# Optimization experiments

Measured on AMD Instinct MI355X. Metric: run time of the kernel, lower is better.

The kernel has to match this reference:

```python
import jax, jax.numpy as jnp
import numpy as np

HID = 2048
NH = 16
HD = HID // NH  # 128
THETA = 10000.0


def _rope_cos_sin(position_ids):
    # inv_freq: [HD/2]
    inv_freq = 1.0 / (THETA ** (jnp.arange(0, HD, 2, dtype=jnp.float32) / HD))
    freqs = position_ids.astype(jnp.float32)[:, :, None] * inv_freq[None, None, :]  # [b,s,hd/2]
    emb = jnp.concatenate([freqs, freqs], axis=-1)  # [b,s,hd]
    return jnp.cos(emb), jnp.sin(emb)


def _rotate_half(x):
    x1, x2 = x[..., : HD // 2], x[..., HD // 2:]
    return jnp.concatenate([-x2, x1], axis=-1)


def setup_inputs() -> dict:
    key = jax.random.key(0)
    ks = jax.random.split(key, 10)
    b, s = 2, 2048
    scale = 1.0 / np.sqrt(HID)
    hidden_states = jax.random.normal(ks[0], (b, s, HID), dtype=jnp.float32)
    wq = jax.random.normal(ks[1], (HID, HID), dtype=jnp.float32) * scale
    wk = jax.random.normal(ks[2], (HID, HID), dtype=jnp.float32) * scale
    wv = jax.random.normal(ks[3], (HID, HID), dtype=jnp.float32) * scale
    wo = jax.random.normal(ks[4], (HID, HID), dtype=jnp.float32) * scale
    bq = jnp.zeros((HID,), jnp.float32)
    bk = jnp.zeros((HID,), jnp.float32)
    bv = jnp.zeros((HID,), jnp.float32)
    bo = jnp.zeros((HID,), jnp.float32)
    # HF-style additive causal mask [b,1,q,kv]: 0 on/below diag, large negative above
    neg = jnp.finfo(jnp.float32).min
    causal = jnp.where(jnp.tril(jnp.ones((s, s), dtype=bool)), 0.0, neg)
    attention_mask = jnp.broadcast_to(causal[None, None], (b, 1, s, s)).astype(jnp.float32)
    position_ids = jnp.broadcast_to(jnp.arange(s, dtype=jnp.int32)[None], (b, s))
    return {
        "hidden_states": hidden_states,
        "wq": wq, "bq": bq, "wk": wk, "bk": bk,
        "wv": wv, "bv": bv, "wo": wo, "bo": bo,
        "attention_mask": attention_mask, "position_ids": position_ids,
    }


def reference(hidden_states, wq, bq, wk, bk, wv, bv, wo, bo, attention_mask, position_ids):
    b, s, _ = hidden_states.shape
    q = hidden_states @ wq.T + bq  # [b,s,hid]
    k = hidden_states @ wk.T + bk
    v = hidden_states @ wv.T + bv
    # [b, nh, s, hd]
    q = q.reshape(b, s, NH, HD).transpose(0, 2, 1, 3)
    k = k.reshape(b, s, NH, HD).transpose(0, 2, 1, 3)
    v = v.reshape(b, s, NH, HD).transpose(0, 2, 1, 3)
    cos, sin = _rope_cos_sin(position_ids)  # [b,s,hd]
    cos, sin = cos[:, None], sin[:, None]  # unsqueeze_dim=1 -> [b,1,s,hd]
    q = q * cos + _rotate_half(q) * sin
    k = k * cos + _rotate_half(k) * sin
    scores = jnp.einsum("bhqd,bhkd->bhqk", q, k) / np.sqrt(HD)
    scores = scores + attention_mask
    attn = jax.nn.softmax(scores.astype(jnp.float32), axis=-1).astype(q.dtype)
    out = jnp.einsum("bhqk,bhkd->bhqd", attn, v)  # [b,nh,s,hd]
    out = out.transpose(0, 2, 1, 3).reshape(b, s, HID)
    return out @ wo.T + bo
```

## Files before the change

### kernel.cpp

```cpp
#include <hip/hip_runtime.h>

#define S_LEN 2048
#define HID   2048
#define NHEAD 16
#define HDIM  128
#define BATCH 2
#define KDIM  2048

using bf16x8  = __attribute__((ext_vector_type(8))) short;
using f32x4   = __attribute__((ext_vector_type(4))) float;
using short4v = __attribute__((ext_vector_type(4))) short;

__device__ __forceinline__ short f2bf(float f) {
  union { float f; unsigned u; } v; v.f = f;
  unsigned r = v.u + 0x7fffu + ((v.u >> 16) & 1u);
  return (short)(r >> 16);
}
__device__ __forceinline__ float bf2f(short s) {
  union { unsigned u; float f; } v;
  v.u = ((unsigned)(unsigned short)s) << 16;
  return v.f;
}

__device__ __forceinline__ void gl_lds16(const void* g, void* l) {
  __builtin_amdgcn_global_load_lds(
      (const __attribute__((address_space(1))) void*)g,
      (__attribute__((address_space(3))) void*)l, 16, 0, 0);
}

__global__ __launch_bounds__(256)
void convert_all(const float* __restrict__ hs, const float* __restrict__ wq,
                 const float* __restrict__ wk, const float* __restrict__ wv,
                 const float* __restrict__ wo,
                 short* __restrict__ hsb, short* __restrict__ wqkv,
                 short* __restrict__ wob)
{
  int i = blockIdx.x * 256 + threadIdx.x;
  const float* src; short* dst; int j = i;
  if (j < 1048576)      { src = hs; dst = hsb; }
  else if (j < 1572864) { j -= 1048576; src = wq; dst = wqkv; }
  else if (j < 2097152) { j -= 1572864; src = wk; dst = wqkv + 4194304; }
  else if (j < 2621440) { j -= 2097152; src = wv; dst = wqkv + 8388608; }
  else                  { j -= 2621440; src = wo; dst = wob; }
  f32x4 a = ((const f32x4*)src)[2 * j];
  f32x4 b = ((const f32x4*)src)[2 * j + 1];
  bf16x8 o;
  o[0]=f2bf(a[0]); o[1]=f2bf(a[1]); o[2]=f2bf(a[2]); o[3]=f2bf(a[3]);
  o[4]=f2bf(b[0]); o[5]=f2bf(b[1]); o[6]=f2bf(b[2]); o[7]=f2bf(b[3]);
  ((bf16x8*)dst)[j] = o;
}

template<int KIND>
__global__ __launch_bounds__(256)
void gemm128(const short* __restrict__ A, const short* __restrict__ B,
             const float* __restrict__ bias0, const float* __restrict__ bias1,
             const float* __restrict__ bias2,
             void* __restrict__ O0, void* __restrict__ O1, void* __restrict__ O2)
{
  __shared__ __align__(16) short As[128 * 64];
  __shared__ __align__(16) short Bs[128 * 64];
  const int tid  = threadIdx.x;
  const int lane = tid & 63, wave = tid >> 6;
  const int ln = lane & 15, g = lane >> 4;
  const int wr = wave >> 1, wc = wave & 1;
  const int m0 = blockIdx.x * 128, n0 = blockIdx.y * 128;

  const int srow   = tid >> 3;
  const int schunk = (tid & 7) ^ (srow & 7);
  const short* aS = A + (size_t)(m0 + srow) * KDIM + schunk * 8;
  const short* bS = B + (size_t)(n0 + srow) * KDIM + schunk * 8;

  f32x4 acc[4][4] = {};

  for (int k0 = 0; k0 < KDIM; k0 += 64) {
    __syncthreads();
#pragma unroll
    for (int j = 0; j < 4; ++j) {
      gl_lds16(aS + k0 + j * (32 * KDIM), &As[j * 2048 + tid * 8]);
      gl_lds16(bS + k0 + j * (32 * KDIM), &Bs[j * 2048 + tid * 8]);
    }
    __syncthreads();

#pragma unroll
    for (int ks = 0; ks < 2; ++ks) {
      bf16x8 af[4], bfm[4];
#pragma unroll
      for (int i = 0; i < 4; ++i) {
        const int r = wr * 64 + i * 16 + ln;
        af[i] = *(const bf16x8*)&As[r * 64 + (((ks * 4 + g) ^ (r & 7)) << 3)];
      }
#pragma unroll
      for (int j2 = 0; j2 < 4; ++j2) {
        const int r = wc * 64 + j2 * 16 + ln;
        bfm[j2] = *(const bf16x8*)&Bs[r * 64 + (((ks * 4 + g) ^ (r & 7)) << 3)];
      }
#pragma unroll
      for (int i = 0; i < 4; ++i)
#pragma unroll
        for (int j2 = 0; j2 < 4; ++j2)
          acc[i][j2] = __builtin_amdgcn_mfma_f32_16x16x32_bf16(af[i], bfm[j2], acc[i][j2], 0, 0, 0);
    }
  }

  if constexpr (KIND == 0) {
    const int seg   = n0 >> 11;
    const int nbase = (n0 & 2047) + wc * 64;
    const float* bias = (seg == 0) ? bias0 : (seg == 1) ? bias1 : bias2;
    float bvv[4];
#pragma unroll
    for (int j = 0; j < 4; ++j) bvv[j] = bias[nbase + j * 16 + ln];
    if (seg < 2) {
      short* C = (short*)(seg ? O1 : O0);
#pragma unroll
      for (int i = 0; i < 4; ++i) {
        const int mb = m0 + wr * 64 + i * 16 + 4 * g;
#pragma unroll
        for (int j = 0; j < 4; ++j) {
          const int nl = nbase + j * 16 + ln;
          const int h = nl >> 7, d = nl & 127;
#pragma unroll
          for (int e = 0; e < 4; ++e) {
            const int m = mb + e, bb = m >> 11, t = m & (S_LEN - 1);
            C[((size_t)((bb * NHEAD + h) * S_LEN + t) << 7) + d] = f2bf(acc[i][j][e] + bvv[j]);
          }
        }
      }
    } else {
      short* C = (short*)O2;
#pragma unroll
      for (int i = 0; i < 4; ++i) {
        const int mb = m0 + wr * 64 + i * 16 + 4 * g;
        const int bb = mb >> 11, t0 = mb & (S_LEN - 1);
#pragma unroll
        for (int j = 0; j < 4; ++j) {
          const int nl = nbase + j * 16 + ln;
          const int h = nl >> 7, d = nl & 127;
          short4v v;
#pragma unroll
          for (int e = 0; e < 4; ++e) v[e] = f2bf(acc[i][j][e] + bvv[j]);
          *(short4v*)&C[((size_t)((bb * NHEAD + h) * HDIM + d)) * S_LEN + t0] = v;
        }
      }
    }
  } else {
    float* C = (float*)O0;
    float bvv[4];
#pragma unroll
    for (int j = 0; j < 4; ++j) bvv[j] = bias0[n0 + wc * 64 + j * 16 + ln];
#pragma unroll
    for (int i = 0; i < 4; ++i) {
      const int mb = m0 + wr * 64 + i * 16 + 4 * g;
#pragma unroll
      for (int j = 0; j < 4; ++j) {
        const int n = n0 + wc * 64 + j * 16 + ln;
#pragma unroll
        for (int e = 0; e < 4; ++e)
          C[(size_t)(mb + e) * HID + n] = acc[i][j][e] + bvv[j];
      }
    }
  }
}

#define QSCALE 0.12752767502f
__global__ __launch_bounds__(256)
void rope_kernel(short* __restrict__ Qb, short* __restrict__ Kb,
                 const int* __restrict__ pos_ids)
{
  const int row = blockIdx.x * 4 + (threadIdx.x >> 6);
  const int d   = threadIdx.x & 63;
  const int bh  = row >> 11, t = row & (S_LEN - 1);
  const int b   = bh >> 4;
  const float pos = (float)pos_ids[b * S_LEN + t];
  const float inv = powf(10000.0f, -(float)d * (1.0f / 64.0f));
  float s, c;
  sincosf(pos * inv, &s, &c);
  const size_t base = (size_t)row * HDIM;
  {
    float x1 = bf2f(Qb[base + d]), x2 = bf2f(Qb[base + d + 64]);
    Qb[base + d]      = f2bf((x1 * c - x2 * s) * QSCALE);
    Qb[base + d + 64] = f2bf((x2 * c + x1 * s) * QSCALE);
  }
  {
    float x1 = bf2f(Kb[base + d]), x2 = bf2f(Kb[base + d + 64]);
    Kb[base + d]      = f2bf(x1 * c - x2 * s);
    Kb[base + d + 64] = f2bf(x2 * c + x1 * s);
  }
}

__global__ __launch_bounds__(512)
void attn_kernel(const short* __restrict__ Qb, const short* __restrict__ Kb,
                 const short* __restrict__ Vt, short* __restrict__ AO)
{
  __shared__ __align__(16) short Ks[64 * 128];
  __shared__ __align__(16) short Vs[128 * 64];
  __shared__ __align__(16) short Ps[8][16 * 64];
  const int tid  = threadIdx.x;
  const int wave = tid >> 6, lane = tid & 63;
  const int ln = lane & 15, g = lane >> 4;
  const int bid = blockIdx.x;
  const int bh  = bid & 31;
  const int grp = bid >> 5;
  const int yt  = (grp & 7) ^ ((grp & 8) ? 15 : 0);
  const int qw  = yt * 128 + wave * 16;

  bf16x8 qf[4];
#pragma unroll
  for (int ks = 0; ks < 4; ++ks)
    qf[ks] = *(const bf16x8*)&Qb[((size_t)bh * S_LEN + qw + ln) * HDIM + ks * 32 + g * 8];

  f32x4 o[8] = {};
  float m_e[4], l_e[4];
#pragma unroll
  for (int e = 0; e < 4; ++e) { m_e[e] = -3.0e38f; l_e[e] = 0.f; }

  const int kvt_max = 2 * yt + 1;
  for (int kvt = 0; kvt <= kvt_max; ++kvt) {
    const int kv0 = kvt * 64;
    __syncthreads();
#pragma unroll
    for (int p = 0; p < 2; ++p) {
      const int gi = tid + p * 512;
      {
        const int row = gi >> 4, c8 = gi & 15;
        bf16x8 v = *(const bf16x8*)&Kb[((size_t)bh * S_LEN + kv0 + row) * HDIM + c8 * 8];
        *(bf16x8*)&Ks[(row * 128 + c8 * 8) ^ ((row & 7) << 3)] = v;
      }
      {
        const int dr = gi >> 3, cg = gi & 7;
        bf16x8 v = *(const bf16x8*)&Vt[((size_t)bh * HDIM + dr) * S_LEN + kv0 + cg * 8];
        *(bf16x8*)&Vs[(dr * 64 + cg * 8) ^ ((dr & 7) << 3)] = v;
      }
    }
    __syncthreads();

    f32x4 sfr[4] = {};
    __builtin_amdgcn_s_setprio(1);
#pragma unroll
    for (int ks = 0; ks < 4; ++ks) {
#pragma unroll
      for (int nt = 0; nt < 4; ++nt) {
        const int row = nt * 16 + ln;
        bf16x8 kf = *(const bf16x8*)&Ks[(row * 128 + ks * 32 + g * 8) ^ ((ln & 7) << 3)];
        sfr[nt] = __builtin_amdgcn_mfma_f32_16x16x32_bf16(qf[ks], kf, sfr[nt], 0, 0, 0);
      }
    }
    __builtin_amdgcn_s_setprio(0);

    float rmax_e[4];
#pragma unroll
    for (int e = 0; e < 4; ++e) {
      const int q = qw + 4 * g + e;
      float rmax = -3.0e38f;
#pragma unroll
      for (int nt = 0; nt < 4; ++nt) {
        float v = sfr[nt][e];
        if (kv0 + nt * 16 + ln > q) v = -3.0e38f;
        sfr[nt][e] = v;
        rmax = fmaxf(rmax, v);
      }
#pragma unroll
      for (int msk = 1; msk < 16; msk <<= 1)
        rmax = fmaxf(rmax, __shfl_xor(rmax, msk));
      rmax_e[e] = rmax;
    }

    bool grow = false;
#pragma unroll
    for (int e = 0; e < 4; ++e) grow |= (rmax_e[e] > m_e[e] + 8.0f);
    if (__any(grow)) {
#pragma unroll
      for (int e = 0; e < 4; ++e) {
        const float nm = fmaxf(m_e[e], rmax_e[e]);
        const float corr = exp2f(m_e[e] - nm);
        m_e[e] = nm;
        l_e[e] *= corr;
#pragma unroll
        for (int nt2 = 0; nt2 < 8; ++nt2) o[nt2][e] *= corr;
      }
    }

#pragma unroll
    for (int e = 0; e < 4; ++e) {
      float psum = 0.f;
#pragma unroll
      for (int nt = 0; nt < 4; ++nt) {
        const float pv = exp2f(sfr[nt][e] - m_e[e]);
        sfr[nt][e] = pv;
        psum += pv;
      }
      l_e[e] += psum;
    }

    short* pw = &Ps[wave][0];
#pragma unroll
    for (int e = 0; e < 4; ++e) {
      const int r = 4 * g + e;
#pragma unroll
      for (int nt = 0; nt < 4; ++nt) {
        const int cc = nt * 16 + ln;
        pw[(r * 64 + cc) ^ ((r & 7) << 3)] = f2bf(sfr[nt][e]);
      }
    }
    asm volatile("s_waitcnt lgkmcnt(0)" ::: "memory");
    __builtin_amdgcn_sched_barrier(0);

    __builtin_amdgcn_s_setprio(1);
#pragma unroll
    for (int ks2 = 0; ks2 < 2; ++ks2) {
      bf16x8 pa = *(const bf16x8*)&pw[(ln * 64 + ks2 * 32 + g * 8) ^ ((ln & 7) << 3)];
#pragma unroll
      for (int nt2 = 0; nt2 < 8; ++nt2) {
        const int row = nt2 * 16 + ln;
        bf16x8 vb = *(const bf16x8*)&Vs[(row * 64 + ks2 * 32 + g * 8) ^ ((ln & 7) << 3)];
        o[nt2] = __builtin_amdgcn_mfma_f32_16x16x32_bf16(pa, vb, o[nt2], 0, 0, 0);
      }
    }
    __builtin_amdgcn_s_setprio(0);
  }

  const int b = bh >> 4, h = bh & 15;
#pragma unroll
  for (int e = 0; e < 4; ++e) {
    float l = l_e[e];
#pragma unroll
    for (int msk = 1; msk < 16; msk <<= 1)
      l += __shfl_xor(l, msk);
    const float inv = 1.0f / l;
    const int q = qw + 4 * g + e;
    short* dst = &AO[((size_t)b * S_LEN + q) * HID + h * HDIM];
#pragma unroll
    for (int nt2 = 0; nt2 < 8; ++nt2)
      dst[nt2 * 16 + ln] = f2bf(o[nt2][e] * inv);
  }
}

extern "C" void kernel_launch(void* const* d_in, const int* in_sizes, int n_in,
                              void* d_out, int out_size, void* d_ws, size_t ws_size,
                              hipStream_t stream)
{
  const float* hs = (const float*)d_in[0];
  const float* wq = (const float*)d_in[1];
  const float* bq = (const float*)d_in[2];
  const float* wk = (const float*)d_in[3];
  const float* bk = (const float*)d_in[4];
  const float* wv = (const float*)d_in[5];
  const float* bv = (const float*)d_in[6];
  const float* wo = (const float*)d_in[7];
  const float* bo = (const float*)d_in[8];
  const int*  pos = (const int*)d_in[10];
  float* out = (float*)d_out;

  const size_t TSZ = (size_t)BATCH * NHEAD * S_LEN * HDIM;
  short* Qb   = (short*)d_ws;
  short* Kb   = Qb + TSZ;
  short* Vt   = Kb + TSZ;
  short* hsb  = Vt + TSZ;
  short* AO   = hsb;
  short* Wqkv = hsb + TSZ;
  short* wob  = Wqkv + 12582912;

  convert_all<<<12288, 256, 0, stream>>>(hs, wq, wk, wv, wo, hsb, Wqkv, wob);
  gemm128<0><<<dim3(32, 48), 256, 0, stream>>>(hsb, Wqkv, bq, bk, bv, Qb, Kb, Vt);
  rope_kernel<<<(BATCH * NHEAD * S_LEN) / 4, 256, 0, stream>>>(Qb, Kb, pos);
  attn_kernel<<<512, 512, 0, stream>>>(Qb, Kb, Vt, AO);
  gemm128<1><<<dim3(32, 16), 256, 0, stream>>>(AO, wob, bo, nullptr, nullptr, out, nullptr, nullptr);
}
```

Baseline: 276.6 us.

## Double-buffer K/V tiles in attention with async global-to-LDS loads

The attention kernel now keeps two LDS buffers for K and V. It prefetches the next KV tile with direct global-to-LDS loads while the current tile is being computed, and uses vmcnt waits plus barriers in place of the synchronous load-then-sync pattern. The XOR swizzle is moved from the LDS destination into the global source address, which leaves the LDS layout unchanged. The aim is to hide global memory latency behind the MFMA work. The cost is double the K/V LDS footprint, which may reduce occupancy.

```diff
diff --git a/kernel.cpp b/kernel.cpp
--- a/kernel.cpp
+++ b/kernel.cpp
@@ -191,8 +191,8 @@
 void attn_kernel(const short* __restrict__ Qb, const short* __restrict__ Kb,
                  const short* __restrict__ Vt, short* __restrict__ AO)
 {
-  __shared__ __align__(16) short Ks[64 * 128];
-  __shared__ __align__(16) short Vs[128 * 64];
+  __shared__ __align__(16) short Ks[2][64 * 128];
+  __shared__ __align__(16) short Vs[2][128 * 64];
   __shared__ __align__(16) short Ps[8][16 * 64];
   const int tid  = threadIdx.x;
   const int wave = tid >> 6, lane = tid & 63;
@@ -203,6 +203,11 @@
   const int yt  = (grp & 7) ^ ((grp & 8) ? 15 : 0);
   const int qw  = yt * 128 + wave * 16;
 
+  const short* Kbh = Kb + (size_t)bh * (S_LEN * HDIM);
+  const short* Vbh = Vt + (size_t)bh * (S_LEN * HDIM);
+  const int kOff = (tid >> 4) * HDIM + (((tid & 15) ^ ((tid >> 4) & 7)) << 3);
+  const int vOff = (tid >> 3) * S_LEN + (((tid & 7) ^ ((tid >> 3) & 7)) << 3);
+
   bf16x8 qf[4];
 #pragma unroll
   for (int ks = 0; ks < 4; ++ks)
@@ -213,25 +218,30 @@
 #pragma unroll
   for (int e = 0; e < 4; ++e) { m_e[e] = -3.0e38f; l_e[e] = 0.f; }
 
+  auto stage = [&](int kvt, int b) {
+    const int kv0 = kvt * 64;
+    const short* ksrc = Kbh + (size_t)kv0 * HDIM + kOff;
+    const short* vsrc = Vbh + kv0 + vOff;
+    gl_lds16(ksrc,                 &Ks[b][tid * 8]);
+    gl_lds16(ksrc + 32 * HDIM,     &Ks[b][4096 + tid * 8]);
+    gl_lds16(vsrc,                 &Vs[b][tid * 8]);
+    gl_lds16(vsrc + 64 * S_LEN,    &Vs[b][4096 + tid * 8]);
+  };
+
+  stage(0, 0);
   const int kvt_max = 2 * yt + 1;
   for (int kvt = 0; kvt <= kvt_max; ++kvt) {
-    const int kv0 = kvt * 64;
-    __syncthreads();
-#pragma unroll
-    for (int p = 0; p < 2; ++p) {
-      const int gi = tid + p * 512;
-      {
-        const int row = gi >> 4, c8 = gi & 15;
-        bf16x8 v = *(const bf16x8*)&Kb[((size_t)bh * S_LEN + kv0 + row) * HDIM + c8 * 8];
-        *(bf16x8*)&Ks[(row * 128 + c8 * 8) ^ ((row & 7) << 3)] = v;
-      }
-      {
-        const int dr = gi >> 3, cg = gi & 7;
-        bf16x8 v = *(const bf16x8*)&Vt[((size_t)bh * HDIM + dr) * S_LEN + kv0 + cg * 8];
-        *(bf16x8*)&Vs[(dr * 64 + cg * 8) ^ ((dr & 7) << 3)] = v;
-      }
-    }
-    __syncthreads();
+    const int cur = kvt & 1;
+    if (kvt < kvt_max) {
+      stage(kvt + 1, cur ^ 1);
+      asm volatile("s_waitcnt vmcnt(4)" ::: "memory");
+    } else {
+      asm volatile("s_waitcnt vmcnt(0)" ::: "memory");
+    }
+    __builtin_amdgcn_s_barrier();
+    __builtin_amdgcn_sched_barrier(0);
+    const short* kb = &Ks[cur][0];
+    const short* vbuf = &Vs[cur][0];
 
     f32x4 sfr[4] = {};
     __builtin_amdgcn_s_setprio(1);
@@ -240,12 +250,13 @@
 #pragma unroll
       for (int nt = 0; nt < 4; ++nt) {
         const int row = nt * 16 + ln;
-        bf16x8 kf = *(const bf16x8*)&Ks[(row * 128 + ks * 32 + g * 8) ^ ((ln & 7) << 3)];
+        bf16x8 kf = *(const bf16x8*)&kb[(row * 128 + ks * 32 + g * 8) ^ ((ln & 7) << 3)];
         sfr[nt] = __builtin_amdgcn_mfma_f32_16x16x32_bf16(qf[ks], kf, sfr[nt], 0, 0, 0);
       }
     }
     __builtin_amdgcn_s_setprio(0);
 
+    const int kv0 = kvt * 64;
     float rmax_e[4];
 #pragma unroll
     for (int e = 0; e < 4; ++e) {
@@ -311,11 +322,14 @@
 #pragma unroll
       for (int nt2 = 0; nt2 < 8; ++nt2) {
         const int row = nt2 * 16 + ln;
-        bf16x8 vb = *(const bf16x8*)&Vs[(row * 64 + ks2 * 32 + g * 8) ^ ((ln & 7) << 3)];
+        bf16x8 vb = *(const bf16x8*)&vbuf[(row * 64 + ks2 * 32 + g * 8) ^ ((row & 7) << 3)];
         o[nt2] = __builtin_amdgcn_mfma_f32_16x16x32_bf16(pa, vb, o[nt2], 0, 0, 0);
       }
     }
     __builtin_amdgcn_s_setprio(0);
+
+    __builtin_amdgcn_sched_barrier(0);
+    __builtin_amdgcn_s_barrier();
   }
 
   const int b = bh >> 4, h = bh & 15;
```

New measurement: 275.4 us. About the same (-0.4%).

## Load 128-row KV tiles via direct global-to-LDS loads; loop convert kernel

Applied to the files above, without the earlier changes.

The attention kernel now stages 128-row K and V tiles per barrier pair using global_load_lds direct copies, with the XOR swizzle applied on the global side. Each tile is processed as two 64-column halves, which halves the number of block-wide synchronisations. The convert kernel launches fewer blocks, each handling six elements in a strided loop, and the RoPE frequency uses exp2f instead of powf. LDS use rises to 64KB for K and V plus the P buffers, which may limit occupancy, and on the diagonal tile the upper half now does fully masked work.

```diff
diff --git a/kernel.cpp b/kernel.cpp
--- a/kernel.cpp
+++ b/kernel.cpp
@@ -35,19 +35,23 @@
                  short* __restrict__ hsb, short* __restrict__ wqkv,
                  short* __restrict__ wob)
 {
-  int i = blockIdx.x * 256 + threadIdx.x;
-  const float* src; short* dst; int j = i;
-  if (j < 1048576)      { src = hs; dst = hsb; }
-  else if (j < 1572864) { j -= 1048576; src = wq; dst = wqkv; }
-  else if (j < 2097152) { j -= 1572864; src = wk; dst = wqkv + 4194304; }
-  else if (j < 2621440) { j -= 2097152; src = wv; dst = wqkv + 8388608; }
-  else                  { j -= 2621440; src = wo; dst = wob; }
-  f32x4 a = ((const f32x4*)src)[2 * j];
-  f32x4 b = ((const f32x4*)src)[2 * j + 1];
-  bf16x8 o;
-  o[0]=f2bf(a[0]); o[1]=f2bf(a[1]); o[2]=f2bf(a[2]); o[3]=f2bf(a[3]);
-  o[4]=f2bf(b[0]); o[5]=f2bf(b[1]); o[6]=f2bf(b[2]); o[7]=f2bf(b[3]);
-  ((bf16x8*)dst)[j] = o;
+  const int base = blockIdx.x * 256 + threadIdx.x;
+#pragma unroll
+  for (int it = 0; it < 6; ++it) {
+    int j = base + it * 524288;
+    const float* src; short* dst;
+    if (j < 1048576)      { src = hs; dst = hsb; }
+    else if (j < 1572864) { j -= 1048576; src = wq; dst = wqkv; }
+    else if (j < 2097152) { j -= 1572864; src = wk; dst = wqkv + 4194304; }
+    else if (j < 2621440) { j -= 2097152; src = wv; dst = wqkv + 8388608; }
+    else                  { j -= 2621440; src = wo; dst = wob; }
+    f32x4 a = ((const f32x4*)src)[2 * j];
+    f32x4 b = ((const f32x4*)src)[2 * j + 1];
+    bf16x8 o;
+    o[0]=f2bf(a[0]); o[1]=f2bf(a[1]); o[2]=f2bf(a[2]); o[3]=f2bf(a[3]);
+    o[4]=f2bf(b[0]); o[5]=f2bf(b[1]); o[6]=f2bf(b[2]); o[7]=f2bf(b[3]);
+    ((bf16x8*)dst)[j] = o;
+  }
 }
 
 template<int KIND>
@@ -171,7 +175,7 @@
   const int bh  = row >> 11, t = row & (S_LEN - 1);
   const int b   = bh >> 4;
   const float pos = (float)pos_ids[b * S_LEN + t];
-  const float inv = powf(10000.0f, -(float)d * (1.0f / 64.0f));
+  const float inv = exp2f((float)d * -0.20762050593f);
   float s, c;
   sincosf(pos * inv, &s, &c);
   const size_t base = (size_t)row * HDIM;
@@ -191,8 +195,8 @@
 void attn_kernel(const short* __restrict__ Qb, const short* __restrict__ Kb,
                  const short* __restrict__ Vt, short* __restrict__ AO)
 {
-  __shared__ __align__(16) short Ks[64 * 128];
-  __shared__ __align__(16) short Vs[128 * 64];
+  __shared__ __align__(16) short Ks[128 * 128];
+  __shared__ __align__(16) short Vs[128 * 128];
   __shared__ __align__(16) short Ps[8][16 * 64];
   const int tid  = threadIdx.x;
   const int wave = tid >> 6, lane = tid & 63;
@@ -203,6 +207,12 @@
   const int yt  = (grp & 7) ^ ((grp & 8) ? 15 : 0);
   const int qw  = yt * 128 + wave * 16;
 
+  const short* Kbh = Kb + (size_t)bh * (S_LEN * HDIM);
+  const short* Vbh = Vt + (size_t)bh * (S_LEN * HDIM);
+  const int sOff = (tid >> 4) * 0 + ((((tid & 15) ^ ((tid >> 4) & 7))) << 3);
+  const int kOff = (tid >> 4) * HDIM  + sOff;
+  const int vOff = (tid >> 4) * S_LEN + sOff;
+
   bf16x8 qf[4];
 #pragma unroll
   for (int ks = 0; ks < 4; ++ks)
@@ -213,112 +223,108 @@
 #pragma unroll
   for (int e = 0; e < 4; ++e) { m_e[e] = -3.0e38f; l_e[e] = 0.f; }
 
-  const int kvt_max = 2 * yt + 1;
-  for (int kvt = 0; kvt <= kvt_max; ++kvt) {
-    const int kv0 = kvt * 64;
+  for (int kvt = 0; kvt <= yt; ++kvt) {
+    const int kv0 = kvt * 128;
     __syncthreads();
 #pragma unroll
-    for (int p = 0; p < 2; ++p) {
-      const int gi = tid + p * 512;
-      {
-        const int row = gi >> 4, c8 = gi & 15;
-        bf16x8 v = *(const bf16x8*)&Kb[((size_t)bh * S_LEN + kv0 + row) * HDIM + c8 * 8];
-        *(bf16x8*)&Ks[(row * 128 + c8 * 8) ^ ((row & 7) << 3)] = v;
-      }
-      {
-        const int dr = gi >> 3, cg = gi & 7;
-        bf16x8 v = *(const bf16x8*)&Vt[((size_t)bh * HDIM + dr) * S_LEN + kv0 + cg * 8];
-        *(bf16x8*)&Vs[(dr * 64 + cg * 8) ^ ((dr & 7) << 3)] = v;
-      }
+    for (int p = 0; p < 4; ++p) {
+      gl_lds16(Kbh + (size_t)kv0 * HDIM + kOff + p * (32 * HDIM),
+               &Ks[p * 4096 + tid * 8]);
+      gl_lds16(Vbh + kv0 + vOff + p * (32 * S_LEN),
+               &Vs[p * 4096 + tid * 8]);
     }
     __syncthreads();
 
-    f32x4 sfr[4] = {};
-    __builtin_amdgcn_s_setprio(1);
-#pragma unroll
-    for (int ks = 0; ks < 4; ++ks) {
-#pragma unroll
-      for (int nt = 0; nt < 4; ++nt) {
-        const int row = nt * 16 + ln;
-        bf16x8 kf = *(const bf16x8*)&Ks[(row * 128 + ks * 32 + g * 8) ^ ((ln & 7) << 3)];
-        sfr[nt] = __builtin_amdgcn_mfma_f32_16x16x32_bf16(qf[ks], kf, sfr[nt], 0, 0, 0);
-      }
-    }
-    __builtin_amdgcn_s_setprio(0);
-
-    float rmax_e[4];
-#pragma unroll
-    for (int e = 0; e < 4; ++e) {
-      const int q = qw + 4 * g + e;
-      float rmax = -3.0e38f;
-#pragma unroll
-      for (int nt = 0; nt < 4; ++nt) {
-        float v = sfr[nt][e];
-        if (kv0 + nt * 16 + ln > q) v = -3.0e38f;
-        sfr[nt][e] = v;
-        rmax = fmaxf(rmax, v);
-      }
-#pragma unroll
-      for (int msk = 1; msk < 16; msk <<= 1)
-        rmax = fmaxf(rmax, __shfl_xor(rmax, msk));
-      rmax_e[e] = rmax;
-    }
-
-    bool grow = false;
-#pragma unroll
-    for (int e = 0; e < 4; ++e) grow |= (rmax_e[e] > m_e[e] + 8.0f);
-    if (__any(grow)) {
+    for (int h = 0; h < 2; ++h) {
+      const int kvb = kv0 + h * 64;
+
+      f32x4 sfr[4] = {};
+      __builtin_amdgcn_s_setprio(1);
+#pragma unroll
+      for (int ks = 0; ks < 4; ++ks) {
+#pragma unroll
+        for (int nt = 0; nt < 4; ++nt) {
+          const int row = h * 64 + nt * 16 + ln;
+          bf16x8 kf = *(const bf16x8*)&Ks[(row * 128 + ks * 32 + g * 8) ^ ((row & 7) << 3)];
+          sfr[nt] = __builtin_amdgcn_mfma_f32_16x16x32_bf16(qf[ks], kf, sfr[nt], 0, 0, 0);
+        }
+      }
+      __builtin_amdgcn_s_setprio(0);
+
+      float rmax_e[4];
 #pragma unroll
       for (int e = 0; e < 4; ++e) {
-        const float nm = fmaxf(m_e[e], rmax_e[e]);
-        const float corr = exp2f(m_e[e] - nm);
-        m_e[e] = nm;
-        l_e[e] *= corr;
-#pragma unroll
-        for (int nt2 = 0; nt2 < 8; ++nt2) o[nt2][e] *= corr;
-      }
-    }
-
-#pragma unroll
-    for (int e = 0; e < 4; ++e) {
-      float psum = 0.f;
-#pragma unroll
-      for (int nt = 0; nt < 4; ++nt) {
-        const float pv = exp2f(sfr[nt][e] - m_e[e]);
-        sfr[nt][e] = pv;
-        psum += pv;
-      }
-      l_e[e] += psum;
-    }
-
-    short* pw = &Ps[wave][0];
-#pragma unroll
-    for (int e = 0; e < 4; ++e) {
-      const int r = 4 * g + e;
-#pragma unroll
-      for (int nt = 0; nt < 4; ++nt) {
-        const int cc = nt * 16 + ln;
-        pw[(r * 64 + cc) ^ ((r & 7) << 3)] = f2bf(sfr[nt][e]);
-      }
-    }
-    asm volatile("s_waitcnt lgkmcnt(0)" ::: "memory");
-    __builtin_amdgcn_sched_barrier(0);
-
-    __builtin_amdgcn_s_setprio(1);
-#pragma unroll
-    for (int ks2 = 0; ks2 < 2; ++ks2) {
-      bf16x8 pa = *(const bf16x8*)&pw[(ln * 64 + ks2 * 32 + g * 8) ^ ((ln & 7) << 3)];
-#pragma unroll
-      for (int nt2 = 0; nt2 < 8; ++nt2) {
-        const int row = nt2 * 16 + ln;
-        bf16x8 vb = *(const bf16x8*)&Vs[(row * 64 + ks2 * 32 + g * 8) ^ ((ln & 7) << 3)];
-        o[nt2] = __builtin_amdgcn_mfma_f32_16x16x32_bf16(pa, vb, o[nt2], 0, 0, 0);
-      }
-    }
-    __builtin_amdgcn_s_setprio(0);
-  }
-
-  const int b = bh >> 4, h = bh & 15;
+        const int q = qw + 4 * g + e;
+        float rmax = -3.0e38f;
+#pragma unroll
+        for (int nt = 0; nt < 4; ++nt) {
+          float v = sfr[nt][e];
+          if (kvb + nt * 16 + ln > q) v = -3.0e38f;
+          sfr[nt][e] = v;
+          rmax = fmaxf(rmax, v);
+        }
+#pragma unroll
+        for (int msk = 1; msk < 16; msk <<= 1)
+          rmax = fmaxf(rmax, __shfl_xor(rmax, msk));
+        rmax_e[e] = rmax;
+      }
+
+      bool grow = false;
+#pragma unroll
+      for (int e = 0; e < 4; ++e) grow |= (rmax_e[e] > m_e[e] + 8.0f);
+      if (__any(grow)) {
+#pragma unroll
+        for (int e = 0; e < 4; ++e) {
+          const float nm = fmaxf(m_e[e], rmax_e[e]);
+          const float corr = exp2f(m_e[e] - nm);
+          m_e[e] = nm;
+          l_e[e] *= corr;
+#pragma unroll
+          for (int nt2 = 0; nt2 < 8; ++nt2) o[nt2][e] *= corr;
+        }
+      }
+
+#pragma unroll
+      for (int e = 0; e < 4; ++e) {
+        float psum = 0.f;
+#pragma unroll
+        for (int nt = 0; nt < 4; ++nt) {
+          const float pv = exp2f(sfr[nt][e] - m_e[e]);
+          sfr[nt][e] = pv;
+          psum += pv;
+        }
+        l_e[e] += psum;
+      }
+
+      short* pw = &Ps[wave][0];
+#pragma unroll
+      for (int e = 0; e < 4; ++e) {
+        const int r = 4 * g + e;
+#pragma unroll
+        for (int nt = 0; nt < 4; ++nt) {
+          const int cc = nt * 16 + ln;
+          pw[(r * 64 + cc) ^ ((r & 7) << 3)] = f2bf(sfr[nt][e]);
+        }
+      }
+      asm volatile("s_waitcnt lgkmcnt(0)" ::: "memory");
+      __builtin_amdgcn_sched_barrier(0);
+
+      __builtin_amdgcn_s_setprio(1);
+#pragma unroll
+      for (int ks2 = 0; ks2 < 2; ++ks2) {
+        bf16x8 pa = *(const bf16x8*)&pw[(ln * 64 + ks2 * 32 + g * 8) ^ ((ln & 7) << 3)];
+#pragma unroll
+        for (int nt2 = 0; nt2 < 8; ++nt2) {
+          const int row = nt2 * 16 + ln;
+          bf16x8 vb = *(const bf16x8*)&Vs[(row * 128 + h * 64 + ks2 * 32 + g * 8) ^ ((row & 7) << 3)];
+          o[nt2] = __builtin_amdgcn_mfma_f32_16x16x32_bf16(pa, vb, o[nt2], 0, 0, 0);
+        }
+      }
+      __builtin_amdgcn_s_setprio(0);
+    }
+  }
+
+  const int b = bh >> 4, h2 = bh & 15;
 #pragma unroll
   for (int e = 0; e < 4; ++e) {
     float l = l_e[e];
@@ -327,7 +333,7 @@
       l += __shfl_xor(l, msk);
     const float inv = 1.0f / l;
     const int q = qw + 4 * g + e;
-    short* dst = &AO[((size_t)b * S_LEN + q) * HID + h * HDIM];
+    short* dst = &AO[((size_t)b * S_LEN + q) * HID + h2 * HDIM];
 #pragma unroll
     for (int nt2 = 0; nt2 < 8; ++nt2)
       dst[nt2 * 16 + ln] = f2bf(o[nt2][e] * inv);
@@ -359,7 +365,7 @@
   short* Wqkv = hsb + TSZ;
   short* wob  = Wqkv + 12582912;
 
-  convert_all<<<12288, 256, 0, stream>>>(hs, wq, wk, wv, wo, hsb, Wqkv, wob);
+  convert_all<<<2048, 256, 0, stream>>>(hs, wq, wk, wv, wo, hsb, Wqkv, wob);
   gemm128<0><<<dim3(32, 48), 256, 0, stream>>>(hsb, Wqkv, bq, bk, bv, Qb, Kb, Vt);
   rope_kernel<<<(BATCH * NHEAD * S_LEN) / 4, 256, 0, stream>>>(Qb, Kb, pos);
   attn_kernel<<<512, 512, 0, stream>>>(Qb, Kb, Vt, AO);
```

Measured after the change: 273.0 us. About the same (-1.3%).
